# Kernel optimization log

Measured on AMD Instinct MI355X. Metric: run time of the kernel, lower is better.

The kernel has to match this reference:

```python
import jax, jax.numpy as jnp
import numpy as np

N_ENT = 4096
N_REL = 4
F = 128
BATCH = 8192
ADJ_DENSITY = 0.01


def setup_inputs() -> dict:
    key = jax.random.key(0)
    ks = jax.random.split(key, 8)
    features = jax.random.normal(ks[0], (N_ENT, F), dtype=jnp.float32)
    # sparse binary adjacency per relation (matches count_nonzero degree normalization)
    adj = (jax.random.uniform(ks[1], (N_REL, N_ENT, N_ENT)) < ADJ_DENSITY).astype(jnp.float32)
    W1 = jax.random.normal(ks[2], (N_REL, F, F), dtype=jnp.float32)  # [R, out, in]
    W2 = jax.random.normal(ks[3], (N_REL, F, F), dtype=jnp.float32)
    # DistMult init: diagonal relation matrices (full params, as in the torch code)
    diag_vals = jax.random.normal(ks[4], (N_REL, F), dtype=jnp.float32)
    relmats = jax.vmap(jnp.diag)(diag_vals)  # [R, F, F]
    e1_idx = jax.random.randint(ks[5], (BATCH,), 0, N_ENT)
    rel_idx = jax.random.randint(ks[6], (BATCH,), 0, N_REL)
    e2_idx = jax.random.randint(ks[7], (BATCH,), 0, N_ENT)
    return {"features": features, "adj": adj, "W1": W1, "W2": W2,
            "relmats": relmats, "e1_idx": e1_idx, "rel_idx": rel_idx, "e2_idx": e2_idx}


def _conv_layer(adj, feat, W):
    # degree normalization: 1 / count_nonzero(A_r, dim=1), zeros -> 1
    deg = jnp.sum(adj != 0, axis=2).astype(feat.dtype)            # [R, N]
    inv_deg = 1.0 / jnp.where(deg == 0, 1.0, deg)                 # [R, N]
    agg = jnp.einsum('rnm,mf->rnf', adj, feat)                    # [R, N, F_in]
    y = jnp.einsum('rnf,rof->rno', agg, W)                        # [R, N, F_out] (x @ W_r.T)
    y = jnp.sum(inv_deg[:, :, None] * y, axis=0)                  # [N, F_out]
    return jax.nn.sigmoid(y)


def reference(features, adj, W1, W2, relmats, e1_idx, rel_idx, e2_idx):
    h = _conv_layer(adj, features, W1)
    h = _conv_layer(adj, h, W2)
    # DistMult scores: pred[r] = h @ M_r @ h.T  -> [R, N, N]
    pred = jnp.einsum('nf,rfg,mg->rnm', h, relmats, h)
    # per-sample scalar gather pred[rel][e1][e2]
    return pred[rel_idx, e1_idx, e2_idx]
```

## Files before the change

### kernel.cpp

```cpp
#include <hip/hip_runtime.h>
#include <hip/hip_bf16.h>

#define N_ENT 4096
#define N_REL 4
#define FDIM 128
#define KDIM 512
#define MAXNZ 128
#define BATCH 8192
#define NROWS (N_REL * N_ENT)

typedef float f4v __attribute__((ext_vector_type(4)));

__global__ __launch_bounds__(256) void k_prep(
    const float* __restrict__ W1, const float* __restrict__ W2,
    const float* __restrict__ M, const float* __restrict__ adj,
    const float* __restrict__ feat,
    float* __restrict__ W1T, float* __restrict__ W2T, float* __restrict__ diagM,
    unsigned short* __restrict__ cols, int* __restrict__ cnt,
    float* __restrict__ inv_deg, float* __restrict__ agg) {
  int blk = blockIdx.x;
  if (blk < NROWS) {
    int row = blk;
    int r = row >> 12;
    int node = row & (N_ENT - 1);
    __shared__ unsigned short sc[MAXNZ];
    __shared__ float part[8][FDIM];
    __shared__ int wtot[4];
    int w = threadIdx.x >> 6;
    int l = threadIdx.x & 63;
    const f4v* rowp = (const f4v*)(adj + (size_t)row * N_ENT);
    unsigned mask = 0;
#pragma unroll
    for (int q = 0; q < 4; ++q) {
      f4v v = __builtin_nontemporal_load(rowp + w * 256 + q * 64 + l);
      if (v.x != 0.f) mask |= 1u << (q * 4 + 0);
      if (v.y != 0.f) mask |= 1u << (q * 4 + 1);
      if (v.z != 0.f) mask |= 1u << (q * 4 + 2);
      if (v.w != 0.f) mask |= 1u << (q * 4 + 3);
    }
    int my = __popc(mask);
    int scan = my;
#pragma unroll
    for (int off = 1; off < 64; off <<= 1) {
      int nb = __shfl_up(scan, off, 64);
      if (l >= off) scan += nb;
    }
    if (l == 63) wtot[w] = scan;
    int excl = scan - my;
    __syncthreads();
    int wbase = 0, c = 0;
#pragma unroll
    for (int ww = 0; ww < 4; ++ww) {
      int t = wtot[ww];
      if (ww < w) wbase += t;
      c += t;
    }
    if (c > MAXNZ) c = MAXNZ;
    int p = wbase + excl;
    unsigned m = mask;
    while (m) {
      int b = __ffs(m) - 1;
      m &= m - 1;
      int col = w * 1024 + (b >> 2) * 256 + l * 4 + (b & 3);
      if (p < MAXNZ) sc[p] = (unsigned short)col;
      ++p;
    }
    __syncthreads();
    float wgt = 1.0f / (float)(c > 0 ? c : 1);
    if (threadIdx.x < c) cols[(size_t)row * MAXNZ + threadIdx.x] = sc[threadIdx.x];
    if (threadIdx.x == 0) { cnt[row] = c; inv_deg[row] = wgt; }
    int ll = threadIdx.x & 31;
    int g = threadIdx.x >> 5;
    const float* fp = feat + ll * 4;
    float ax = 0.f, ay = 0.f, az = 0.f, aw = 0.f;
    int j = g;
    for (; j + 8 < c; j += 16) {
      float4 v0 = *(const float4*)(fp + (int)sc[j] * FDIM);
      float4 v1 = *(const float4*)(fp + (int)sc[j + 8] * FDIM);
      ax += v0.x + v1.x; ay += v0.y + v1.y;
      az += v0.z + v1.z; aw += v0.w + v1.w;
    }
    if (j < c) {
      float4 v = *(const float4*)(fp + (int)sc[j] * FDIM);
      ax += v.x; ay += v.y; az += v.z; aw += v.w;
    }
    part[g][ll * 4 + 0] = ax; part[g][ll * 4 + 1] = ay;
    part[g][ll * 4 + 2] = az; part[g][ll * 4 + 3] = aw;
    __syncthreads();
    if (threadIdx.x < FDIM) {
      float s = 0.f;
#pragma unroll
      for (int gg = 0; gg < 8; ++gg) s += part[gg][threadIdx.x];
      agg[(size_t)node * KDIM + r * FDIM + threadIdx.x] = s * wgt;
    }
    return;
  }
  int ab = blk - NROWS;
  if (ab < 512) {
    int id = ab * 256 + threadIdx.x;
    int which = id >> 16;
    int e = id & 65535;
    int rr = e >> 14, rem = e & 16383, ff = rem >> 7, o = rem & 127;
    const float* srcw = which ? W2 : W1;
    float* dst = which ? W2T : W1T;
    dst[e] = srcw[(rr * FDIM + o) * FDIM + ff];
    return;
  }
  int idx = (ab - 512) * 256 + threadIdx.x;
  int rr = idx >> 7, ff = idx & 127;
  diagM[idx] = M[((size_t)(rr * FDIM + ff)) * FDIM + ff];
}

__device__ __forceinline__ void gemm_body(
    const float* __restrict__ A, const float* __restrict__ B,
    float* __restrict__ C, int n0, float (*red)[128]) {
  constexpr int KD = KDIM, KH = KDIM / 2, Ncol = FDIM;
  int o = threadIdx.x & 127;
  int half = threadIdx.x >> 7;
  const float* Ap = A + (size_t)n0 * KD + half * KH;
  const float* Bp = B + (size_t)half * KH * Ncol + o;
  float acc[8] = {0.f, 0.f, 0.f, 0.f, 0.f, 0.f, 0.f, 0.f};
#pragma unroll 2
  for (int k = 0; k < KH; k += 4) {
    float4 a0 = *(const float4*)(Ap + 0 * KD + k);
    float4 a1 = *(const float4*)(Ap + 1 * KD + k);
    float4 a2 = *(const float4*)(Ap + 2 * KD + k);
    float4 a3 = *(const float4*)(Ap + 3 * KD + k);
    float4 a4 = *(const float4*)(Ap + 4 * KD + k);
    float4 a5 = *(const float4*)(Ap + 5 * KD + k);
    float4 a6 = *(const float4*)(Ap + 6 * KD + k);
    float4 a7 = *(const float4*)(Ap + 7 * KD + k);
    float b0 = Bp[(size_t)(k + 0) * Ncol];
    float b1 = Bp[(size_t)(k + 1) * Ncol];
    float b2 = Bp[(size_t)(k + 2) * Ncol];
    float b3 = Bp[(size_t)(k + 3) * Ncol];
    acc[0] += a0.x * b0 + a0.y * b1 + a0.z * b2 + a0.w * b3;
    acc[1] += a1.x * b0 + a1.y * b1 + a1.z * b2 + a1.w * b3;
    acc[2] += a2.x * b0 + a2.y * b1 + a2.z * b2 + a2.w * b3;
    acc[3] += a3.x * b0 + a3.y * b1 + a3.z * b2 + a3.w * b3;
    acc[4] += a4.x * b0 + a4.y * b1 + a4.z * b2 + a4.w * b3;
    acc[5] += a5.x * b0 + a5.y * b1 + a5.z * b2 + a5.w * b3;
    acc[6] += a6.x * b0 + a6.y * b1 + a6.z * b2 + a6.w * b3;
    acc[7] += a7.x * b0 + a7.y * b1 + a7.z * b2 + a7.w * b3;
  }
  if (half) {
#pragma unroll
    for (int i = 0; i < 8; ++i) red[i][o] = acc[i];
  }
  __syncthreads();
  if (!half) {
#pragma unroll
    for (int i = 0; i < 8; ++i) {
      float v = acc[i] + red[i][o];
      v = 1.f / (1.f + __expf(-v));
      C[(size_t)(n0 + i) * Ncol + o] = v;
    }
  }
}

__global__ __launch_bounds__(256) void k_gemm(
    const float* __restrict__ A, const float* __restrict__ B,
    float* __restrict__ C) {
  __shared__ float red[8][128];
  gemm_body(A, B, C, blockIdx.x * 8, red);
}

__global__ __launch_bounds__(256) void k_layer2(
    const unsigned short* __restrict__ cols, const int* __restrict__ cnt,
    const float* __restrict__ inv_deg, const float* __restrict__ h1,
    const float* __restrict__ W2T, float* __restrict__ h2) {
  int n0 = blockIdx.x * 4;
  __shared__ unsigned short lc[4][N_REL][MAXNZ];
  __shared__ __align__(16) float aggL[4][KDIM];
  __shared__ float red[4][128];
  {
    int i = threadIdx.x >> 4;
    int t16 = threadIdx.x & 15;
    int nb = i >> 2, r = i & 3;
    int row = r * N_ENT + n0 + nb;
    int c = cnt[row];
    for (int j = t16; j < c; j += 16)
      lc[nb][r][j] = cols[(size_t)row * MAXNZ + j];
  }
  __syncthreads();
  {
    int l = threadIdx.x & 31;
    int g = threadIdx.x >> 5;
    const float* fp = h1 + l * 4;
#pragma unroll
    for (int q = 0; q < 2; ++q) {
      int pair = g + q * 8;
      int nb = pair >> 2, r = pair & 3;
      int row = r * N_ENT + n0 + nb;
      int c = cnt[row];
      float w = inv_deg[row];
      float ax = 0.f, ay = 0.f, az = 0.f, aw = 0.f;
      int j = 0;
      for (; j + 2 <= c; j += 2) {
        float4 v0 = *(const float4*)(fp + (int)lc[nb][r][j] * FDIM);
        float4 v1 = *(const float4*)(fp + (int)lc[nb][r][j + 1] * FDIM);
        ax += v0.x + v1.x; ay += v0.y + v1.y;
        az += v0.z + v1.z; aw += v0.w + v1.w;
      }
      if (j < c) {
        float4 v = *(const float4*)(fp + (int)lc[nb][r][j] * FDIM);
        ax += v.x; ay += v.y; az += v.z; aw += v.w;
      }
      float4 res; res.x = ax * w; res.y = ay * w; res.z = az * w; res.w = aw * w;
      *(float4*)&aggL[nb][r * FDIM + l * 4] = res;
    }
  }
  __syncthreads();
  {
    constexpr int KH = KDIM / 2, Ncol = FDIM;
    int o = threadIdx.x & 127;
    int half = threadIdx.x >> 7;
    const float* Bp = W2T + (size_t)half * KH * Ncol + o;
    int kbase = half * KH;
    float acc[4] = {0.f, 0.f, 0.f, 0.f};
#pragma unroll 2
    for (int k = 0; k < KH; k += 4) {
      float4 a0 = *(const float4*)&aggL[0][kbase + k];
      float4 a1 = *(const float4*)&aggL[1][kbase + k];
      float4 a2 = *(const float4*)&aggL[2][kbase + k];
      float4 a3 = *(const float4*)&aggL[3][kbase + k];
      float b0 = Bp[(size_t)(k + 0) * Ncol];
      float b1 = Bp[(size_t)(k + 1) * Ncol];
      float b2 = Bp[(size_t)(k + 2) * Ncol];
      float b3 = Bp[(size_t)(k + 3) * Ncol];
      acc[0] += a0.x * b0 + a0.y * b1 + a0.z * b2 + a0.w * b3;
      acc[1] += a1.x * b0 + a1.y * b1 + a1.z * b2 + a1.w * b3;
      acc[2] += a2.x * b0 + a2.y * b1 + a2.z * b2 + a2.w * b3;
      acc[3] += a3.x * b0 + a3.y * b1 + a3.z * b2 + a3.w * b3;
    }
    if (half) {
#pragma unroll
      for (int i = 0; i < 4; ++i) red[i][o] = acc[i];
    }
    __syncthreads();
    if (!half) {
#pragma unroll
      for (int i = 0; i < 4; ++i) {
        float v = acc[i] + red[i][o];
        v = 1.f / (1.f + __expf(-v));
        h2[(size_t)(n0 + i) * Ncol + o] = v;
      }
    }
  }
}

__global__ __launch_bounds__(256) void k_score(
    const float* __restrict__ h, const float* __restrict__ diagM,
    const int* __restrict__ e1, const int* __restrict__ rel,
    const int* __restrict__ e2, float* __restrict__ out) {
  int wave = threadIdx.x >> 6;
  int lane = threadIdx.x & 63;
  int b = blockIdx.x * 4 + wave;
  int a = e1[b], r = rel[b], c = e2[b];
  const float* hp = h + (size_t)a * FDIM;
  const float* dp = diagM + (size_t)r * FDIM;
  const float* gp = h + (size_t)c * FDIM;
  float v = hp[lane] * dp[lane] * gp[lane]
          + hp[lane + 64] * dp[lane + 64] * gp[lane + 64];
#pragma unroll
  for (int off = 32; off > 0; off >>= 1) v += __shfl_down(v, off, 64);
  if (lane == 0) out[b] = v;
}

extern "C" void kernel_launch(void* const* d_in, const int* in_sizes, int n_in,
                              void* d_out, int out_size, void* d_ws, size_t ws_size,
                              hipStream_t stream) {
  const float* feat = (const float*)d_in[0];
  const float* adj  = (const float*)d_in[1];
  const float* W1   = (const float*)d_in[2];
  const float* W2   = (const float*)d_in[3];
  const float* M    = (const float*)d_in[4];
  const int* e1     = (const int*)d_in[5];
  const int* rel    = (const int*)d_in[6];
  const int* e2     = (const int*)d_in[7];
  float* out = (float*)d_out;

  char* ws = (char*)d_ws;
  unsigned short* cols = (unsigned short*)(ws);
  int*   cnt  = (int*)  (ws + 4194304);
  float* inv  = (float*)(ws + 4259840);
  float* W1T  = (float*)(ws + 4325376);
  float* W2T  = (float*)(ws + 4587520);
  float* dM   = (float*)(ws + 4849664);
  float* agg  = (float*)(ws + 5111808);
  float* h1   = (float*)(ws + 13500416);
  float* h2   = (float*)(ws + 15597568);

  k_prep<<<NROWS + 514, 256, 0, stream>>>(
      W1, W2, M, adj, feat, W1T, W2T, dM, cols, cnt, inv, agg);

  k_gemm<<<N_ENT / 8, 256, 0, stream>>>(agg, W1T, h1);
  k_layer2<<<N_ENT / 4, 256, 0, stream>>>(cols, cnt, inv, h1, W2T, h2);
  k_score<<<BATCH / 4, 256, 0, stream>>>(h2, dM, e1, rel, e2, out);
}
```

Before: 432.4 us.

## Move layer-1 aggregation out of prep into fused gather-GEMM layer kernel

The adjacency-scan kernel now only extracts column indices and degree counts, writing columns directly to global memory instead of staging them in shared memory. Layer-1 aggregation and its GEMM are fused into a new k_layer1 kernel that shares a templated body with layer 2, so the 8 MB intermediate agg buffer is no longer written and re-read. This costs an extra read of the column lists from global memory, and the prep kernel loses the gather work it used to overlap with the adjacency streaming.

```diff
diff --git a/kernel.cpp b/kernel.cpp
--- a/kernel.cpp
+++ b/kernel.cpp
@@ -11,20 +11,15 @@
 
 typedef float f4v __attribute__((ext_vector_type(4)));
 
-__global__ __launch_bounds__(256) void k_prep(
+__global__ __launch_bounds__(256) void k_sparse(
     const float* __restrict__ W1, const float* __restrict__ W2,
     const float* __restrict__ M, const float* __restrict__ adj,
-    const float* __restrict__ feat,
     float* __restrict__ W1T, float* __restrict__ W2T, float* __restrict__ diagM,
     unsigned short* __restrict__ cols, int* __restrict__ cnt,
-    float* __restrict__ inv_deg, float* __restrict__ agg) {
+    float* __restrict__ inv_deg) {
   int blk = blockIdx.x;
   if (blk < NROWS) {
     int row = blk;
-    int r = row >> 12;
-    int node = row & (N_ENT - 1);
-    __shared__ unsigned short sc[MAXNZ];
-    __shared__ float part[8][FDIM];
     __shared__ int wtot[4];
     int w = threadIdx.x >> 6;
     int l = threadIdx.x & 63;
@@ -58,40 +53,17 @@
     if (c > MAXNZ) c = MAXNZ;
     int p = wbase + excl;
     unsigned m = mask;
+    unsigned short* cp = cols + (size_t)row * MAXNZ;
     while (m) {
       int b = __ffs(m) - 1;
       m &= m - 1;
       int col = w * 1024 + (b >> 2) * 256 + l * 4 + (b & 3);
-      if (p < MAXNZ) sc[p] = (unsigned short)col;
+      if (p < MAXNZ) cp[p] = (unsigned short)col;
       ++p;
     }
-    __syncthreads();
-    float wgt = 1.0f / (float)(c > 0 ? c : 1);
-    if (threadIdx.x < c) cols[(size_t)row * MAXNZ + threadIdx.x] = sc[threadIdx.x];
-    if (threadIdx.x == 0) { cnt[row] = c; inv_deg[row] = wgt; }
-    int ll = threadIdx.x & 31;
-    int g = threadIdx.x >> 5;
-    const float* fp = feat + ll * 4;
-    float ax = 0.f, ay = 0.f, az = 0.f, aw = 0.f;
-    int j = g;
-    for (; j + 8 < c; j += 16) {
-      float4 v0 = *(const float4*)(fp + (int)sc[j] * FDIM);
-      float4 v1 = *(const float4*)(fp + (int)sc[j + 8] * FDIM);
-      ax += v0.x + v1.x; ay += v0.y + v1.y;
-      az += v0.z + v1.z; aw += v0.w + v1.w;
-    }
-    if (j < c) {
-      float4 v = *(const float4*)(fp + (int)sc[j] * FDIM);
-      ax += v.x; ay += v.y; az += v.z; aw += v.w;
-    }
-    part[g][ll * 4 + 0] = ax; part[g][ll * 4 + 1] = ay;
-    part[g][ll * 4 + 2] = az; part[g][ll * 4 + 3] = aw;
-    __syncthreads();
-    if (threadIdx.x < FDIM) {
-      float s = 0.f;
-#pragma unroll
-      for (int gg = 0; gg < 8; ++gg) s += part[gg][threadIdx.x];
-      agg[(size_t)node * KDIM + r * FDIM + threadIdx.x] = s * wgt;
+    if (threadIdx.x == 0) {
+      cnt[row] = c;
+      inv_deg[row] = 1.0f / (float)(c > 0 ? c : 1);
     }
     return;
   }
@@ -111,68 +83,17 @@
   diagM[idx] = M[((size_t)(rr * FDIM + ff)) * FDIM + ff];
 }
 
-__device__ __forceinline__ void gemm_body(
-    const float* __restrict__ A, const float* __restrict__ B,
-    float* __restrict__ C, int n0, float (*red)[128]) {
-  constexpr int KD = KDIM, KH = KDIM / 2, Ncol = FDIM;
-  int o = threadIdx.x & 127;
-  int half = threadIdx.x >> 7;
-  const float* Ap = A + (size_t)n0 * KD + half * KH;
-  const float* Bp = B + (size_t)half * KH * Ncol + o;
-  float acc[8] = {0.f, 0.f, 0.f, 0.f, 0.f, 0.f, 0.f, 0.f};
-#pragma unroll 2
-  for (int k = 0; k < KH; k += 4) {
-    float4 a0 = *(const float4*)(Ap + 0 * KD + k);
-    float4 a1 = *(const float4*)(Ap + 1 * KD + k);
-    float4 a2 = *(const float4*)(Ap + 2 * KD + k);
-    float4 a3 = *(const float4*)(Ap + 3 * KD + k);
-    float4 a4 = *(const float4*)(Ap + 4 * KD + k);
-    float4 a5 = *(const float4*)(Ap + 5 * KD + k);
-    float4 a6 = *(const float4*)(Ap + 6 * KD + k);
-    float4 a7 = *(const float4*)(Ap + 7 * KD + k);
-    float b0 = Bp[(size_t)(k + 0) * Ncol];
-    float b1 = Bp[(size_t)(k + 1) * Ncol];
-    float b2 = Bp[(size_t)(k + 2) * Ncol];
-    float b3 = Bp[(size_t)(k + 3) * Ncol];
-    acc[0] += a0.x * b0 + a0.y * b1 + a0.z * b2 + a0.w * b3;
-    acc[1] += a1.x * b0 + a1.y * b1 + a1.z * b2 + a1.w * b3;
-    acc[2] += a2.x * b0 + a2.y * b1 + a2.z * b2 + a2.w * b3;
-    acc[3] += a3.x * b0 + a3.y * b1 + a3.z * b2 + a3.w * b3;
-    acc[4] += a4.x * b0 + a4.y * b1 + a4.z * b2 + a4.w * b3;
-    acc[5] += a5.x * b0 + a5.y * b1 + a5.z * b2 + a5.w * b3;
-    acc[6] += a6.x * b0 + a6.y * b1 + a6.z * b2 + a6.w * b3;
-    acc[7] += a7.x * b0 + a7.y * b1 + a7.z * b2 + a7.w * b3;
-  }
-  if (half) {
-#pragma unroll
-    for (int i = 0; i < 8; ++i) red[i][o] = acc[i];
-  }
-  __syncthreads();
-  if (!half) {
-#pragma unroll
-    for (int i = 0; i < 8; ++i) {
-      float v = acc[i] + red[i][o];
-      v = 1.f / (1.f + __expf(-v));
-      C[(size_t)(n0 + i) * Ncol + o] = v;
-    }
-  }
-}
-
-__global__ __launch_bounds__(256) void k_gemm(
-    const float* __restrict__ A, const float* __restrict__ B,
-    float* __restrict__ C) {
-  __shared__ float red[8][128];
-  gemm_body(A, B, C, blockIdx.x * 8, red);
-}
-
-__global__ __launch_bounds__(256) void k_layer2(
+struct LSmem {
+  float aggL[4][KDIM];
+  unsigned short lc[4][N_REL][MAXNZ];
+  float red[4][FDIM];
+};
+
+__device__ __forceinline__ void layer_body(
+    LSmem& S,
     const unsigned short* __restrict__ cols, const int* __restrict__ cnt,
-    const float* __restrict__ inv_deg, const float* __restrict__ h1,
-    const float* __restrict__ W2T, float* __restrict__ h2) {
-  int n0 = blockIdx.x * 4;
-  __shared__ unsigned short lc[4][N_REL][MAXNZ];
-  __shared__ __align__(16) float aggL[4][KDIM];
-  __shared__ float red[4][128];
+    const float* __restrict__ inv_deg, const float* __restrict__ src,
+    const float* __restrict__ BT, float* __restrict__ dst, int n0) {
   {
     int i = threadIdx.x >> 4;
     int t16 = threadIdx.x & 15;
@@ -180,13 +101,13 @@
     int row = r * N_ENT + n0 + nb;
     int c = cnt[row];
     for (int j = t16; j < c; j += 16)
-      lc[nb][r][j] = cols[(size_t)row * MAXNZ + j];
+      S.lc[nb][r][j] = cols[(size_t)row * MAXNZ + j];
   }
   __syncthreads();
   {
     int l = threadIdx.x & 31;
     int g = threadIdx.x >> 5;
-    const float* fp = h1 + l * 4;
+    const float* fp = src + l * 4;
 #pragma unroll
     for (int q = 0; q < 2; ++q) {
       int pair = g + q * 8;
@@ -197,17 +118,17 @@
       float ax = 0.f, ay = 0.f, az = 0.f, aw = 0.f;
       int j = 0;
       for (; j + 2 <= c; j += 2) {
-        float4 v0 = *(const float4*)(fp + (int)lc[nb][r][j] * FDIM);
-        float4 v1 = *(const float4*)(fp + (int)lc[nb][r][j + 1] * FDIM);
+        float4 v0 = *(const float4*)(fp + (int)S.lc[nb][r][j] * FDIM);
+        float4 v1 = *(const float4*)(fp + (int)S.lc[nb][r][j + 1] * FDIM);
         ax += v0.x + v1.x; ay += v0.y + v1.y;
         az += v0.z + v1.z; aw += v0.w + v1.w;
       }
       if (j < c) {
-        float4 v = *(const float4*)(fp + (int)lc[nb][r][j] * FDIM);
+        float4 v = *(const float4*)(fp + (int)S.lc[nb][r][j] * FDIM);
         ax += v.x; ay += v.y; az += v.z; aw += v.w;
       }
       float4 res; res.x = ax * w; res.y = ay * w; res.z = az * w; res.w = aw * w;
-      *(float4*)&aggL[nb][r * FDIM + l * 4] = res;
+      *(float4*)&S.aggL[nb][r * FDIM + l * 4] = res;
     }
   }
   __syncthreads();
@@ -215,15 +136,15 @@
     constexpr int KH = KDIM / 2, Ncol = FDIM;
     int o = threadIdx.x & 127;
     int half = threadIdx.x >> 7;
-    const float* Bp = W2T + (size_t)half * KH * Ncol + o;
+    const float* Bp = BT + (size_t)half * KH * Ncol + o;
     int kbase = half * KH;
     float acc[4] = {0.f, 0.f, 0.f, 0.f};
 #pragma unroll 2
     for (int k = 0; k < KH; k += 4) {
-      float4 a0 = *(const float4*)&aggL[0][kbase + k];
-      float4 a1 = *(const float4*)&aggL[1][kbase + k];
-      float4 a2 = *(const float4*)&aggL[2][kbase + k];
-      float4 a3 = *(const float4*)&aggL[3][kbase + k];
+      float4 a0 = *(const float4*)&S.aggL[0][kbase + k];
+      float4 a1 = *(const float4*)&S.aggL[1][kbase + k];
+      float4 a2 = *(const float4*)&S.aggL[2][kbase + k];
+      float4 a3 = *(const float4*)&S.aggL[3][kbase + k];
       float b0 = Bp[(size_t)(k + 0) * Ncol];
       float b1 = Bp[(size_t)(k + 1) * Ncol];
       float b2 = Bp[(size_t)(k + 2) * Ncol];
@@ -235,18 +156,34 @@
     }
     if (half) {
 #pragma unroll
-      for (int i = 0; i < 4; ++i) red[i][o] = acc[i];
+      for (int i = 0; i < 4; ++i) S.red[i][o] = acc[i];
     }
     __syncthreads();
     if (!half) {
 #pragma unroll
       for (int i = 0; i < 4; ++i) {
-        float v = acc[i] + red[i][o];
+        float v = acc[i] + S.red[i][o];
         v = 1.f / (1.f + __expf(-v));
-        h2[(size_t)(n0 + i) * Ncol + o] = v;
+        dst[(size_t)(n0 + i) * Ncol + o] = v;
       }
     }
   }
+}
+
+__global__ __launch_bounds__(256) void k_layer1(
+    const unsigned short* __restrict__ cols, const int* __restrict__ cnt,
+    const float* __restrict__ inv_deg, const float* __restrict__ feat,
+    const float* __restrict__ W1T, float* __restrict__ h1) {
+  __shared__ __align__(16) LSmem S;
+  layer_body(S, cols, cnt, inv_deg, feat, W1T, h1, blockIdx.x * 4);
+}
+
+__global__ __launch_bounds__(256) void k_layer2(
+    const unsigned short* __restrict__ cols, const int* __restrict__ cnt,
+    const float* __restrict__ inv_deg, const float* __restrict__ h1,
+    const float* __restrict__ W2T, float* __restrict__ h2) {
+  __shared__ __align__(16) LSmem S;
+  layer_body(S, cols, cnt, inv_deg, h1, W2T, h2, blockIdx.x * 4);
 }
 
 __global__ __launch_bounds__(256) void k_score(
@@ -287,14 +224,12 @@
   float* W1T  = (float*)(ws + 4325376);
   float* W2T  = (float*)(ws + 4587520);
   float* dM   = (float*)(ws + 4849664);
-  float* agg  = (float*)(ws + 5111808);
   float* h1   = (float*)(ws + 13500416);
   float* h2   = (float*)(ws + 15597568);
 
-  k_prep<<<NROWS + 514, 256, 0, stream>>>(
-      W1, W2, M, adj, feat, W1T, W2T, dM, cols, cnt, inv, agg);
-
-  k_gemm<<<N_ENT / 8, 256, 0, stream>>>(agg, W1T, h1);
+  k_sparse<<<NROWS + 514, 256, 0, stream>>>(
+      W1, W2, M, adj, W1T, W2T, dM, cols, cnt, inv);
+  k_layer1<<<N_ENT / 4, 256, 0, stream>>>(cols, cnt, inv, feat, W1T, h1);
   k_layer2<<<N_ENT / 4, 256, 0, stream>>>(cols, cnt, inv, h1, W2T, h2);
   k_score<<<BATCH / 4, 256, 0, stream>>>(h2, dM, e1, rel, e2, out);
 }
```

After: 410.1 us. 1.05x faster.
